# Performance work log

Measured on AMD Instinct MI355X. Metric: run time of the kernel, lower is better.

## Reference

```python
import jax, jax.numpy as jnp
import numpy as np

B, S, D = 4, 2048, 768
H = 12
HD = D // H
SCALE = HD ** -0.5


def setup_inputs() -> dict:
    key = jax.random.key(0)
    ks = jax.random.split(key, 5)
    std = D ** -0.5
    return {
        "hidden_states": jax.random.normal(ks[0], (B, S, D), dtype=jnp.float32),
        "qkv_w": jax.random.normal(ks[1], (3 * D, D), dtype=jnp.float32) * std,
        "qkv_b": jnp.zeros((3 * D,), dtype=jnp.float32),
        "proj_w": jax.random.normal(ks[2], (D, D), dtype=jnp.float32) * std,
        "proj_b": jnp.zeros((D,), dtype=jnp.float32),
    }


def reference(hidden_states, qkv_w, qkv_b, proj_w, proj_b):
    b, s, d = hidden_states.shape
    # fused QKV projection: [b,s,3d] -> [3,b,H,s,hd]
    mixed = hidden_states @ qkv_w.T + qkv_b
    mixed = mixed.reshape(b, s, 3, H, HD).transpose(2, 0, 3, 1, 4)
    q, k, v = mixed[0], mixed[1], mixed[2]
    # naive attention: full [b,H,s,s] score matrix, as in original module
    scores = jnp.einsum("bhqd,bhkd->bhqk", q, k) * SCALE
    probs = jax.nn.softmax(scores, axis=-1)
    ctx = jnp.einsum("bhqk,bhkd->bhqd", probs, v)
    ctx = ctx.transpose(0, 2, 1, 3).reshape(b, s, d)
    out = ctx @ proj_w.T + proj_b
    return out
```

## Files before the change

### kernel.cpp

```cpp
#include <hip/hip_runtime.h>
#include <hip/hip_bf16.h>

using short8   = __attribute__((ext_vector_type(8))) short;
using floatx4  = __attribute__((ext_vector_type(4))) float;
using floatx16 = __attribute__((ext_vector_type(16))) float;

#define KDIM 768
#define QSCALE 0.18033688011112042f
#define N1 (8192 * 768)
#define N2 (2304 * 768)
#define N3 (768 * 768)

__device__ __forceinline__ short f2bf(float f) {
    union { float f; unsigned u; } v; v.f = f;
    unsigned r = v.u + 0x7fffu + ((v.u >> 16) & 1u);
    return (short)(r >> 16);
}

__device__ __forceinline__ unsigned pack2bf(float a, float b) {
    __hip_bfloat162 h = __float22bfloat162_rn(float2{a, b});
    union { __hip_bfloat162 h; unsigned u; } c; c.h = h;
    return c.u;
}

__device__ __forceinline__ float fast_exp2(float x) {
#if __has_builtin(__builtin_amdgcn_exp2f)
    return __builtin_amdgcn_exp2f(x);
#else
    return exp2f(x);
#endif
}

__device__ __forceinline__ void async16(const void* g, void* l) {
    __builtin_amdgcn_global_load_lds((const __attribute__((address_space(1))) void*)g,
                                     (__attribute__((address_space(3))) void*)l, 16, 0, 0);
}

__global__ void cvt_all(const float* __restrict__ a, const float* __restrict__ b,
                        const float* __restrict__ c, short* __restrict__ oa,
                        short* __restrict__ ob, short* __restrict__ oc) {
    int i = (blockIdx.x * blockDim.x + threadIdx.x) * 4;
    const float* src; short* dst;
    if (i < N1)            { src = a + i;            dst = oa + i; }
    else if (i < N1 + N2)  { src = b + (i - N1);     dst = ob + (i - N1); }
    else if (i < N1+N2+N3) { src = c + (i - N1 - N2); dst = oc + (i - N1 - N2); }
    else return;
    float4 v = *(const float4*)src;
    short4 o;
    o.x = f2bf(v.x); o.y = f2bf(v.y); o.z = f2bf(v.z); o.w = f2bf(v.w);
    *(short4*)dst = o;
}

__global__ __launch_bounds__(256) void gemm_qkv(
    const short* __restrict__ X, const short* __restrict__ W,
    const float* __restrict__ bias,
    short* __restrict__ Qb, short* __restrict__ Kb, short* __restrict__ Vb)
{
    __shared__ short As[128 * 32];
    __shared__ short Bs[128 * 32];
    int tid = threadIdx.x;
    int w = tid >> 6, l = tid & 63;
    int lane16 = l & 15, quad = l >> 4;
    int wm = w & 1, wn = w >> 1;

    int fid = blockIdx.x + 18 * blockIdx.y;
    int c = fid & 7, s = fid >> 3;
    int my = c * 8 + s / 18;
    int nx = s % 18;
    int m0 = my * 128, n0 = nx * 128;

    floatx4 acc[4][4] = {};

    int srow = w * 32 + (l >> 2);
    int scol = (l & 3) * 8;
    const short* Xg = X + (size_t)(m0 + srow) * KDIM + scol;
    const short* Wg = W + (size_t)(n0 + srow) * KDIM + scol;
    short* AsW = As + (w * 32) * 32;
    short* BsW = Bs + (w * 32) * 32;

    for (int kb = 0; kb < KDIM; kb += 32) {
        __syncthreads();
        async16(Xg + kb,              AsW);
        async16(Xg + kb + 16 * KDIM,  AsW + 16 * 32);
        async16(Wg + kb,              BsW);
        async16(Wg + kb + 16 * KDIM,  BsW + 16 * 32);
        __syncthreads();
        short8 a[4], b[4];
#pragma unroll
        for (int mt = 0; mt < 4; mt++) a[mt] = *(const short8*)(As + (wm * 64 + mt * 16 + lane16) * 32 + quad * 8);
#pragma unroll
        for (int nt = 0; nt < 4; nt++) b[nt] = *(const short8*)(Bs + (wn * 64 + nt * 16 + lane16) * 32 + quad * 8);
#pragma unroll
        for (int mt = 0; mt < 4; mt++)
#pragma unroll
            for (int nt = 0; nt < 4; nt++)
                acc[mt][nt] = __builtin_amdgcn_mfma_f32_16x16x32_bf16(a[mt], b[nt], acc[mt][nt], 0, 0, 0);
    }

#pragma unroll
    for (int mt = 0; mt < 4; mt++) {
        int row = m0 + wm * 64 + mt * 16 + quad * 4;
#pragma unroll
        for (int nt = 0; nt < 4; nt++) {
            int col = n0 + wn * 64 + nt * 16 + lane16;
            int qkv = (col >= 1536) ? 2 : ((col >= 768) ? 1 : 0);
            int rem = col - qkv * 768;
            int h = rem >> 6, e = rem & 63;
            short* dst = (qkv == 0) ? Qb : ((qkv == 1) ? Kb : Vb);
            float sc = (qkv == 0) ? (float)QSCALE : 1.0f;
            float bv = bias[col];
#pragma unroll
            for (int r = 0; r < 4; r++) {
                int i  = row + r;
                int b_ = i >> 11, s_ = i & 2047;
                dst[(((size_t)(b_ * 12 + h)) * 2048 + s_) * 64 + e] = f2bf((acc[mt][nt][r] + bv) * sc);
            }
        }
    }
}

__global__ __launch_bounds__(256) void transpose_v(
    const short* __restrict__ Vb, short* __restrict__ Vt)
{
    __shared__ short T[64 * 66];
    int tid = threadIdx.x;
    int s0 = blockIdx.x * 64, bh = blockIdx.y;
    const short* src = Vb + (size_t)bh * 2048 * 64;
    short* dst = Vt + (size_t)bh * 64 * 2048;

#pragma unroll
    for (int i = 0; i < 2; i++) {
        int slot = i * 256 + tid;
        int s_loc = slot >> 3, ec = slot & 7;
        short8 v = *(const short8*)(src + (size_t)(s0 + s_loc) * 64 + ec * 8);
        *(short8*)(T + s_loc * 66 + ec * 8) = v;
    }
    __syncthreads();
#pragma unroll
    for (int i = 0; i < 2; i++) {
        int slot = i * 256 + tid;
        int e_loc = slot >> 3, sc = slot & 7;
        short8 o;
#pragma unroll
        for (int j = 0; j < 8; j++) {
            int p = sc * 8 + j;
            int kp = (p & 0x33) | ((p & 4) << 1) | ((p & 8) >> 1);
            o[j] = T[kp * 66 + e_loc];
        }
        *(short8*)(dst + (size_t)e_loc * 2048 + s0 + sc * 8) = o;
    }
}

__global__ __launch_bounds__(256, 3) void attn(
    const short* __restrict__ Qb, const short* __restrict__ Kb,
    const short* __restrict__ Vt, short* __restrict__ Ctx)
{
    __shared__ short Ks[512 * 8];
    __shared__ short Vs[512 * 8];
    int tid = threadIdx.x, w = tid >> 6, l = tid & 63;
    int l32 = l & 31, half = l >> 5;

    int fid = blockIdx.x + (blockIdx.y << 4);
    int c = fid & 7, sfl = fid >> 3;
    int bh = c * 6 + (sfl >> 4);
    int qt = sfl & 15;

    const short* Qh  = Qb + (size_t)bh * 2048 * 64;
    const short* Kh  = Kb + (size_t)bh * 2048 * 64;
    const short* Vth = Vt + (size_t)bh * 64 * 2048;
    int qbase = qt * 128 + w * 32;

    const short* kSrc[2];
    const short* vSrc[2];
    short* kDst[2];
    short* vDst[2];
#pragma unroll
    for (int i = 0; i < 2; i++) {
        int slot = i * 256 + tid;
        int row = slot >> 3;
        int g = (slot & 7) ^ (row & 7);
        kSrc[i] = Kh + (size_t)row * 64 + g * 8;
        vSrc[i] = Vth + (size_t)row * 2048 + g * 8;
        kDst[i] = Ks + (size_t)(i * 256 + w * 64) * 8;
        vDst[i] = Vs + (size_t)(i * 256 + w * 64) * 8;
    }

    short8 qf[4];
#pragma unroll
    for (int ks = 0; ks < 4; ks++)
        qf[ks] = *(const short8*)(Qh + (size_t)(qbase + l32) * 64 + ks * 16 + half * 8);

    float lsum = 0.f;
    floatx16 acc[2] = {};
    int sw = l32 & 7;

    for (int kt = 0; kt < 32; kt++) {
        __syncthreads();
#pragma unroll
        for (int i = 0; i < 2; i++) {
            async16(kSrc[i] + (size_t)kt * 64 * 64, kDst[i]);
            async16(vSrc[i] + (size_t)kt * 64,      vDst[i]);
        }
        __syncthreads();

        floatx16 s[2];
        __builtin_amdgcn_s_setprio(1);
#pragma unroll
        for (int nt = 0; nt < 2; nt++) {
            floatx16 cacc = {};
            int rowb = (nt * 32 + l32) * 8;
#pragma unroll
            for (int ks = 0; ks < 4; ks++) {
                short8 kf = *(const short8*)(Ks + (size_t)(rowb + ((ks * 2 + half) ^ sw)) * 8);
                cacc = __builtin_amdgcn_mfma_f32_32x32x16_bf16(kf, qf[ks], cacc, 0, 0, 0);
            }
            s[nt] = cacc;
        }
        __builtin_amdgcn_s_setprio(0);

        union { short8 s8; unsigned u[4]; } pa[4];
#pragma unroll
        for (int nt = 0; nt < 2; nt++)
#pragma unroll
            for (int r = 0; r < 16; r += 2) {
                float p0 = fast_exp2(s[nt][r]);
                float p1 = fast_exp2(s[nt][r + 1]);
                lsum += p0 + p1;
                pa[2 * nt + (r >> 3)].u[(r & 7) >> 1] = pack2bf(p0, p1);
            }

        __builtin_amdgcn_s_setprio(1);
#pragma unroll
        for (int nt = 0; nt < 2; nt++) {
            int rowb = (nt * 32 + l32) * 8;
#pragma unroll
            for (int ks = 0; ks < 4; ks++) {
                short8 vf = *(const short8*)(Vs + (size_t)(rowb + ((ks * 2 + half) ^ sw)) * 8);
                acc[nt] = __builtin_amdgcn_mfma_f32_32x32x16_bf16(pa[ks].s8, vf, acc[nt], 0, 0, 0);
            }
        }
        __builtin_amdgcn_s_setprio(0);
    }

    float denom = lsum + __shfl_xor(lsum, 32);
    float inv_self = 1.0f / denom;

    int b_ = bh / 12, h = bh % 12;
#pragma unroll
    for (int nt = 0; nt < 2; nt++)
#pragma unroll
        for (int r = 0; r < 16; r++) {
            int qloc = (r & 3) + 8 * (r >> 2) + 4 * half;
            float invq = __shfl(inv_self, qloc);
            int q = qbase + qloc;
            int e = nt * 32 + l32;
            Ctx[((size_t)(b_ * 2048 + q)) * 768 + h * 64 + e] = f2bf(acc[nt][r] * invq);
        }
}

__global__ __launch_bounds__(256) void gemm_out(
    const short* __restrict__ Ctx, const short* __restrict__ W,
    const float* __restrict__ bias, float* __restrict__ out)
{
    __shared__ short As[64 * 32];
    __shared__ short Bs[128 * 32];
    int tid = threadIdx.x;
    int w = tid >> 6, l = tid & 63;
    int lane16 = l & 15, quad = l >> 4;
    int wm = w & 1, wn = w >> 1;

    int fid = blockIdx.x + 6 * blockIdx.y;
    int c = fid & 7, s = fid >> 3;
    int my = c * 16 + s / 6;
    int nx = s % 6;
    int m0 = my * 64, n0 = nx * 128;

    floatx4 acc[2][4] = {};

    int srow = tid >> 2;
    int scol = (tid & 3) * 8;
    const short* Xg = Ctx + (size_t)(m0 + srow) * KDIM + scol;
    const short* Wg = W + (size_t)(n0 + srow) * KDIM + scol;
    short* AsW = As + (w * 16) * 32;
    short* BsW = Bs + (w * 16) * 32;

    for (int kb = 0; kb < KDIM; kb += 32) {
        __syncthreads();
        async16(Xg + kb,             AsW);
        async16(Wg + kb,             BsW);
        async16(Wg + kb + 64 * KDIM, BsW + 64 * 32);
        __syncthreads();
        short8 a[2], b[4];
#pragma unroll
        for (int mt = 0; mt < 2; mt++) a[mt] = *(const short8*)(As + (wm * 32 + mt * 16 + lane16) * 32 + quad * 8);
#pragma unroll
        for (int nt = 0; nt < 4; nt++) b[nt] = *(const short8*)(Bs + (wn * 64 + nt * 16 + lane16) * 32 + quad * 8);
#pragma unroll
        for (int mt = 0; mt < 2; mt++)
#pragma unroll
            for (int nt = 0; nt < 4; nt++)
                acc[mt][nt] = __builtin_amdgcn_mfma_f32_16x16x32_bf16(a[mt], b[nt], acc[mt][nt], 0, 0, 0);
    }

#pragma unroll
    for (int mt = 0; mt < 2; mt++) {
        int row = m0 + wm * 32 + mt * 16 + quad * 4;
#pragma unroll
        for (int nt = 0; nt < 4; nt++) {
            int col = n0 + wn * 64 + nt * 16 + lane16;
            float bv = bias[col];
#pragma unroll
            for (int r = 0; r < 4; r++)
                out[(size_t)(row + r) * 768 + col] = acc[mt][nt][r] + bv;
        }
    }
}

extern "C" void kernel_launch(void* const* d_in, const int* in_sizes, int n_in,
                              void* d_out, int out_size, void* d_ws, size_t ws_size,
                              hipStream_t stream) {
    const float* hs     = (const float*)d_in[0];
    const float* qkv_w  = (const float*)d_in[1];
    const float* qkv_b  = (const float*)d_in[2];
    const float* proj_w = (const float*)d_in[3];
    const float* proj_b = (const float*)d_in[4];
    float* out = (float*)d_out;

    short* Xb  = (short*)d_ws;
    short* W1b = Xb  + (size_t)8192 * 768;
    short* W2b = W1b + (size_t)2304 * 768;
    short* Qb  = W2b + (size_t)768 * 768;
    short* Kb  = Qb  + (size_t)8192 * 768;
    short* Vb  = Kb  + (size_t)8192 * 768;
    short* Ctx = Vb  + (size_t)8192 * 768;
    short* Vt  = Xb;

    int ntot = (N1 + N2 + N3) / 4;
    cvt_all<<<(ntot + 255) / 256, 256, 0, stream>>>(hs, qkv_w, proj_w, Xb, W1b, W2b);

    gemm_qkv<<<dim3(18, 64), 256, 0, stream>>>(Xb, W1b, qkv_b, Qb, Kb, Vb);
    transpose_v<<<dim3(32, 48), 256, 0, stream>>>(Vb, Vt);
    attn<<<dim3(16, 48), 256, 0, stream>>>(Qb, Kb, Vt, Ctx);
    gemm_out<<<dim3(6, 128), 256, 0, stream>>>(Ctx, W2b, proj_b, out);
}
```

Measured before the change: 223.3 us.

## Triple-buffer K/V tiles in attention with async prefetch two tiles ahead

Replaces the single-buffered K/V LDS tiles, which needed two barriers per iteration, with a three-slot ring buffer. Tiles are prefetched two iterations ahead, and a vmcnt wait plus a single barrier gates each iteration. This is meant to hide global-to-LDS load latency behind MFMA work. It triples the LDS footprint (48KB), which may reduce occupancy under launch_bounds(256,3).

Measured after the change: 224.7 us. Within noise of the previous version (+0.6%).

```diff
diff --git a/kernel.cpp b/kernel.cpp
--- a/kernel.cpp
+++ b/kernel.cpp
@@ -155,8 +155,8 @@
     const short* __restrict__ Qb, const short* __restrict__ Kb,
     const short* __restrict__ Vt, short* __restrict__ Ctx)
 {
-    __shared__ short Ks[512 * 8];
-    __shared__ short Vs[512 * 8];
+    __shared__ short Ks[3][512 * 8];
+    __shared__ short Vs[3][512 * 8];
     int tid = threadIdx.x, w = tid >> 6, l = tid & 63;
     int l32 = l & 31, half = l >> 5;
 
@@ -172,8 +172,7 @@
 
     const short* kSrc[2];
     const short* vSrc[2];
-    short* kDst[2];
-    short* vDst[2];
+    int dOff[2];
 #pragma unroll
     for (int i = 0; i < 2; i++) {
         int slot = i * 256 + tid;
@@ -181,27 +180,47 @@
         int g = (slot & 7) ^ (row & 7);
         kSrc[i] = Kh + (size_t)row * 64 + g * 8;
         vSrc[i] = Vth + (size_t)row * 2048 + g * 8;
-        kDst[i] = Ks + (size_t)(i * 256 + w * 64) * 8;
-        vDst[i] = Vs + (size_t)(i * 256 + w * 64) * 8;
+        dOff[i] = (i * 256 + w * 64) * 8;
     }
 
     short8 qf[4];
 #pragma unroll
     for (int ks = 0; ks < 4; ks++)
         qf[ks] = *(const short8*)(Qh + (size_t)(qbase + l32) * 64 + ks * 16 + half * 8);
+
+#pragma unroll
+    for (int i = 0; i < 2; i++) {
+        async16(kSrc[i],                  &Ks[0][0] + dOff[i]);
+        async16(vSrc[i],                  &Vs[0][0] + dOff[i]);
+    }
+#pragma unroll
+    for (int i = 0; i < 2; i++) {
+        async16(kSrc[i] + 4096,           &Ks[1][0] + dOff[i]);
+        async16(vSrc[i] + 64,             &Vs[1][0] + dOff[i]);
+    }
 
     float lsum = 0.f;
     floatx16 acc[2] = {};
     int sw = l32 & 7;
 
+    int cur = 0;
     for (int kt = 0; kt < 32; kt++) {
-        __syncthreads();
-#pragma unroll
-        for (int i = 0; i < 2; i++) {
-            async16(kSrc[i] + (size_t)kt * 64 * 64, kDst[i]);
-            async16(vSrc[i] + (size_t)kt * 64,      vDst[i]);
-        }
-        __syncthreads();
+        if (kt < 31) { asm volatile("s_waitcnt vmcnt(4)" ::: "memory"); }
+        else         { asm volatile("s_waitcnt vmcnt(0)" ::: "memory"); }
+        __builtin_amdgcn_s_barrier();
+
+        int pf = kt + 2;
+        if (pf < 32) {
+            int pb = cur >= 1 ? cur - 1 : cur + 2;
+#pragma unroll
+            for (int i = 0; i < 2; i++) {
+                async16(kSrc[i] + (size_t)pf * 4096, &Ks[pb][0] + dOff[i]);
+                async16(vSrc[i] + (size_t)pf * 64,   &Vs[pb][0] + dOff[i]);
+            }
+        }
+
+        const short* Kcur = &Ks[cur][0];
+        const short* Vcur = &Vs[cur][0];
 
         floatx16 s[2];
         __builtin_amdgcn_s_setprio(1);
@@ -211,7 +230,7 @@
             int rowb = (nt * 32 + l32) * 8;
 #pragma unroll
             for (int ks = 0; ks < 4; ks++) {
-                short8 kf = *(const short8*)(Ks + (size_t)(rowb + ((ks * 2 + half) ^ sw)) * 8);
+                short8 kf = *(const short8*)(Kcur + (size_t)(rowb + ((ks * 2 + half) ^ sw)) * 8);
                 cacc = __builtin_amdgcn_mfma_f32_32x32x16_bf16(kf, qf[ks], cacc, 0, 0, 0);
             }
             s[nt] = cacc;
@@ -235,11 +254,13 @@
             int rowb = (nt * 32 + l32) * 8;
 #pragma unroll
             for (int ks = 0; ks < 4; ks++) {
-                short8 vf = *(const short8*)(Vs + (size_t)(rowb + ((ks * 2 + half) ^ sw)) * 8);
+                short8 vf = *(const short8*)(Vcur + (size_t)(rowb + ((ks * 2 + half) ^ sw)) * 8);
                 acc[nt] = __builtin_amdgcn_mfma_f32_32x32x16_bf16(pa[ks].s8, vf, acc[nt], 0, 0, 0);
             }
         }
         __builtin_amdgcn_s_setprio(0);
+
+        cur = (cur == 2) ? 0 : cur + 1;
     }
 
     float denom = lsum + __shfl_xor(lsum, 32);
```

## Give each attention wave two query subtiles to reuse K/V fragments

Applied to the files above, without the earlier changes.

The attention kernel goes from 4 waves of 32 queries each to 2 waves of 64 queries each, keeping the 128-query tile per block. Each wave loads K and V fragments from shared memory once per key tile and applies them to two query groups, which halves LDS reads per MFMA. In exchange, register pressure roughly doubles (two accumulator sets, two P tiles, cached K/V fragments), occupancy hints drop, and each thread issues more async copies per tile.

New measurement: 279.8 us. +25.3%, slower.

```diff
diff --git a/kernel.cpp b/kernel.cpp
--- a/kernel.cpp
+++ b/kernel.cpp
@@ -151,7 +151,7 @@
     }
 }
 
-__global__ __launch_bounds__(256, 3) void attn(
+__global__ __launch_bounds__(128, 2) void attn(
     const short* __restrict__ Qb, const short* __restrict__ Kb,
     const short* __restrict__ Vt, short* __restrict__ Ctx)
 {
@@ -168,94 +168,138 @@
     const short* Qh  = Qb + (size_t)bh * 2048 * 64;
     const short* Kh  = Kb + (size_t)bh * 2048 * 64;
     const short* Vth = Vt + (size_t)bh * 64 * 2048;
-    int qbase = qt * 128 + w * 32;
-
-    const short* kSrc[2];
-    const short* vSrc[2];
-    short* kDst[2];
-    short* vDst[2];
-#pragma unroll
-    for (int i = 0; i < 2; i++) {
-        int slot = i * 256 + tid;
+    int qbase = qt * 128 + w * 64;
+
+    const short* kSrc[4];
+    const short* vSrc[4];
+    short* kDst[4];
+    short* vDst[4];
+#pragma unroll
+    for (int i = 0; i < 4; i++) {
+        int slot = i * 128 + tid;
         int row = slot >> 3;
         int g = (slot & 7) ^ (row & 7);
         kSrc[i] = Kh + (size_t)row * 64 + g * 8;
         vSrc[i] = Vth + (size_t)row * 2048 + g * 8;
-        kDst[i] = Ks + (size_t)(i * 256 + w * 64) * 8;
-        vDst[i] = Vs + (size_t)(i * 256 + w * 64) * 8;
-    }
-
-    short8 qf[4];
-#pragma unroll
-    for (int ks = 0; ks < 4; ks++)
-        qf[ks] = *(const short8*)(Qh + (size_t)(qbase + l32) * 64 + ks * 16 + half * 8);
-
-    float lsum = 0.f;
-    floatx16 acc[2] = {};
+        kDst[i] = Ks + (size_t)(i * 128 + w * 64) * 8;
+        vDst[i] = Vs + (size_t)(i * 128 + w * 64) * 8;
+    }
+
+    short8 qf[2][4];
+#pragma unroll
+    for (int qg = 0; qg < 2; qg++)
+#pragma unroll
+        for (int ks = 0; ks < 4; ks++)
+            qf[qg][ks] = *(const short8*)(Qh + (size_t)(qbase + qg * 32 + l32) * 64 + ks * 16 + half * 8);
+
+    float lsum0 = 0.f, lsum1 = 0.f;
+    floatx16 acc[2][2] = {};
     int sw = l32 & 7;
 
+    union upa { short8 s8; unsigned u[4]; };
+
     for (int kt = 0; kt < 32; kt++) {
         __syncthreads();
 #pragma unroll
-        for (int i = 0; i < 2; i++) {
+        for (int i = 0; i < 4; i++) {
             async16(kSrc[i] + (size_t)kt * 64 * 64, kDst[i]);
             async16(vSrc[i] + (size_t)kt * 64,      vDst[i]);
         }
         __syncthreads();
 
+        short8 kf[2][4];
+#pragma unroll
+        for (int nt = 0; nt < 2; nt++) {
+            int rowb = (nt * 32 + l32) * 8;
+#pragma unroll
+            for (int ks = 0; ks < 4; ks++)
+                kf[nt][ks] = *(const short8*)(Ks + (size_t)(rowb + ((ks * 2 + half) ^ sw)) * 8);
+        }
+
         floatx16 s[2];
         __builtin_amdgcn_s_setprio(1);
-#pragma unroll
-        for (int nt = 0; nt < 2; nt++) {
-            floatx16 cacc = {};
-            int rowb = (nt * 32 + l32) * 8;
+        {
+            floatx16 c0 = {}, c1 = {};
 #pragma unroll
             for (int ks = 0; ks < 4; ks++) {
-                short8 kf = *(const short8*)(Ks + (size_t)(rowb + ((ks * 2 + half) ^ sw)) * 8);
-                cacc = __builtin_amdgcn_mfma_f32_32x32x16_bf16(kf, qf[ks], cacc, 0, 0, 0);
-            }
-            s[nt] = cacc;
+                c0 = __builtin_amdgcn_mfma_f32_32x32x16_bf16(kf[0][ks], qf[0][ks], c0, 0, 0, 0);
+                c1 = __builtin_amdgcn_mfma_f32_32x32x16_bf16(kf[1][ks], qf[0][ks], c1, 0, 0, 0);
+            }
+            s[0] = c0; s[1] = c1;
         }
         __builtin_amdgcn_s_setprio(0);
 
-        union { short8 s8; unsigned u[4]; } pa[4];
+        upa pa0[4], pa1[4];
 #pragma unroll
         for (int nt = 0; nt < 2; nt++)
 #pragma unroll
             for (int r = 0; r < 16; r += 2) {
                 float p0 = fast_exp2(s[nt][r]);
                 float p1 = fast_exp2(s[nt][r + 1]);
-                lsum += p0 + p1;
-                pa[2 * nt + (r >> 3)].u[(r & 7) >> 1] = pack2bf(p0, p1);
+                lsum0 += p0 + p1;
+                pa0[2 * nt + (r >> 3)].u[(r & 7) >> 1] = pack2bf(p0, p1);
             }
 
         __builtin_amdgcn_s_setprio(1);
-#pragma unroll
-        for (int nt = 0; nt < 2; nt++) {
-            int rowb = (nt * 32 + l32) * 8;
+        {
+            floatx16 c0 = {}, c1 = {};
 #pragma unroll
             for (int ks = 0; ks < 4; ks++) {
-                short8 vf = *(const short8*)(Vs + (size_t)(rowb + ((ks * 2 + half) ^ sw)) * 8);
-                acc[nt] = __builtin_amdgcn_mfma_f32_32x32x16_bf16(pa[ks].s8, vf, acc[nt], 0, 0, 0);
-            }
+                c0 = __builtin_amdgcn_mfma_f32_32x32x16_bf16(kf[0][ks], qf[1][ks], c0, 0, 0, 0);
+                c1 = __builtin_amdgcn_mfma_f32_32x32x16_bf16(kf[1][ks], qf[1][ks], c1, 0, 0, 0);
+            }
+            s[0] = c0; s[1] = c1;
         }
         __builtin_amdgcn_s_setprio(0);
-    }
-
-    float denom = lsum + __shfl_xor(lsum, 32);
-    float inv_self = 1.0f / denom;
+
+#pragma unroll
+        for (int nt = 0; nt < 2; nt++)
+#pragma unroll
+            for (int r = 0; r < 16; r += 2) {
+                float p0 = fast_exp2(s[nt][r]);
+                float p1 = fast_exp2(s[nt][r + 1]);
+                lsum1 += p0 + p1;
+                pa1[2 * nt + (r >> 3)].u[(r & 7) >> 1] = pack2bf(p0, p1);
+            }
+
+        short8 vf[2][4];
+#pragma unroll
+        for (int ent = 0; ent < 2; ent++) {
+            int rowb = (ent * 32 + l32) * 8;
+#pragma unroll
+            for (int ks = 0; ks < 4; ks++)
+                vf[ent][ks] = *(const short8*)(Vs + (size_t)(rowb + ((ks * 2 + half) ^ sw)) * 8);
+        }
+
+        __builtin_amdgcn_s_setprio(1);
+#pragma unroll
+        for (int ent = 0; ent < 2; ent++)
+#pragma unroll
+            for (int ks = 0; ks < 4; ks++) {
+                acc[ent][0] = __builtin_amdgcn_mfma_f32_32x32x16_bf16(pa0[ks].s8, vf[ent][ks], acc[ent][0], 0, 0, 0);
+                acc[ent][1] = __builtin_amdgcn_mfma_f32_32x32x16_bf16(pa1[ks].s8, vf[ent][ks], acc[ent][1], 0, 0, 0);
+            }
+        __builtin_amdgcn_s_setprio(0);
+    }
+
+    float den0 = lsum0 + __shfl_xor(lsum0, 32);
+    float den1 = lsum1 + __shfl_xor(lsum1, 32);
+    float inv0 = 1.0f / den0;
+    float inv1 = 1.0f / den1;
 
     int b_ = bh / 12, h = bh % 12;
 #pragma unroll
-    for (int nt = 0; nt < 2; nt++)
-#pragma unroll
-        for (int r = 0; r < 16; r++) {
-            int qloc = (r & 3) + 8 * (r >> 2) + 4 * half;
-            float invq = __shfl(inv_self, qloc);
-            int q = qbase + qloc;
-            int e = nt * 32 + l32;
-            Ctx[((size_t)(b_ * 2048 + q)) * 768 + h * 64 + e] = f2bf(acc[nt][r] * invq);
-        }
+    for (int qg = 0; qg < 2; qg++)
+#pragma unroll
+        for (int ent = 0; ent < 2; ent++)
+#pragma unroll
+            for (int r = 0; r < 16; r++) {
+                int qloc = (r & 3) + 8 * (r >> 2) + 4 * half;
+                float invq = __shfl(qg ? inv1 : inv0, qloc);
+                int q = qbase + qg * 32 + qloc;
+                int e = ent * 32 + l32;
+                Ctx[((size_t)(b_ * 2048 + q)) * 768 + h * 64 + e] = f2bf(acc[ent][qg][r] * invq);
+            }
 }
 
 __global__ __launch_bounds__(256) void gemm_out(
@@ -340,6 +384,6 @@
 
     gemm_qkv<<<dim3(18, 64), 256, 0, stream>>>(Xb, W1b, qkv_b, Qb, Kb, Vb);
     transpose_v<<<dim3(32, 48), 256, 0, stream>>>(Vb, Vt);
-    attn<<<dim3(16, 48), 256, 0, stream>>>(Qb, Kb, Vt, Ctx);
+    attn<<<dim3(16, 48), 128, 0, stream>>>(Qb, Kb, Vt, Ctx);
     gemm_out<<<dim3(6, 128), 256, 0, stream>>>(Ctx, W2b, proj_b, out);
 }
```
